# Optimization experiments

Measured on AMD Instinct MI355X. Metric: run time of the kernel, lower is better.

## Reference

```python
import jax, jax.numpy as jnp
import numpy as np
import math

NUM_HEADS = 16
ROPE_BASE = 10000.0


def _rope_tables(T, head_dim, dtype=jnp.float32):
    pos = jnp.arange(T, dtype=jnp.float32)
    inv_freq = 1.0 / (ROPE_BASE ** (jnp.arange(0, head_dim, 2, dtype=jnp.float32) / head_dim))
    ang = pos[:, None] * inv_freq[None, :]  # (T, D/2)
    return jnp.cos(ang).astype(dtype), jnp.sin(ang).astype(dtype)


def _apply_rope(x, cos, sin):
    # x: (B, T, H, D); rotate interleaved pairs, position indexed along T
    B, T, H, D = x.shape
    xr = x.reshape(B, T, H, D // 2, 2)
    xe, xo = xr[..., 0], xr[..., 1]
    c = cos[None, :, None, :]  # (1, T, 1, D/2)
    s = sin[None, :, None, :]
    re = xe * c - xo * s
    im = xe * s + xo * c
    return jnp.stack([re, im], axis=-1).reshape(B, T, H, D)


def setup_inputs() -> dict:
    key = jax.random.key(0)
    k1, k2, k3 = jax.random.split(key, 3)
    B, T, C = 2, 2048, 1024
    x = jax.random.normal(k1, (B, T, C), dtype=jnp.float32)
    w_qkv = jax.random.normal(k2, (C, 3 * C), dtype=jnp.float32) * (1.0 / math.sqrt(C))
    w_out = jax.random.normal(k3, (C, C), dtype=jnp.float32) * (1.0 / math.sqrt(C))
    return {"x": x, "w_qkv": w_qkv, "w_out": w_out}


def reference(x, w_qkv, w_out):
    B, T, C = x.shape
    H = NUM_HEADS
    D = C // H
    qkv = jnp.einsum('btc,cf->btf', x, w_qkv)  # (B, T, 3C)
    q, k, v = jnp.split(qkv, 3, axis=-1)
    q = q.reshape(B, T, H, D)
    k = k.reshape(B, T, H, D)
    v = v.reshape(B, T, H, D)
    cos, sin = _rope_tables(T, D)
    q = _apply_rope(q, cos, sin)
    k = _apply_rope(k, cos, sin)
    # (B, H, T, T) scores with causal mask
    att = jnp.einsum('bqhd,bkhd->bhqk', q, k) * (1.0 / math.sqrt(D))
    causal = jnp.tril(jnp.ones((T, T), dtype=bool))
    att = jnp.where(causal[None, None], att, -jnp.inf)
    att = jax.nn.softmax(att, axis=-1)
    out = jnp.einsum('bhqk,bkhd->bqhd', att, v).reshape(B, T, C)
    return jnp.einsum('btc,cd->btd', out, w_out)
```

## Files before the change

### kernel.cpp

```cpp
#include <hip/hip_runtime.h>
#include <stdint.h>


#define B_ 2
#define T_ 2048
#define C_ 1024
#define H_ 16
#define D_ 64
#define F_ 3072
#define M_ 4096

typedef unsigned short u16;
typedef unsigned int u32;
typedef u16 u16x2 __attribute__((ext_vector_type(2)));
typedef u16 u16x4 __attribute__((ext_vector_type(4)));
typedef u16 u16x8 __attribute__((ext_vector_type(8)));
typedef __bf16 bf16x4 __attribute__((ext_vector_type(4)));
typedef __bf16 bf16x8 __attribute__((ext_vector_type(8)));
typedef float f32x4 __attribute__((ext_vector_type(4)));

__device__ __forceinline__ float b2f(u16 u) {
  union { unsigned int i; float f; } v; v.i = ((unsigned int)u) << 16; return v.f;
}
__device__ __forceinline__ u16 f2b(float f) {
  unsigned int u = __float_as_uint(f);
  u += 0x7fffu + ((u >> 16) & 1u);
  return (u16)(u >> 16);
}
__device__ __forceinline__ bf16x8 u2b8(u16x8 v) {
  union { u16x8 u; bf16x8 b; } x; x.u = v; return x.b;
}


__global__ __launch_bounds__(256) void rope_table_kernel(float* cosT, float* sinT) {
  int idx = blockIdx.x * 256 + threadIdx.x;
  int t = idx >> 5, i = idx & 31;
  float inv_freq = powf(10000.0f, -(float)(2 * i) / 64.0f);
  float ang = (float)t * inv_freq;
  cosT[idx] = cosf(ang);
  sinT[idx] = sinf(ang);
}

__global__ __launch_bounds__(256) void cast_x_kernel(const float* __restrict__ x,
                                                     u16* __restrict__ xb) {
  int i = blockIdx.x * 256 + threadIdx.x;
  float4 v = ((const float4*)x)[i];
  u16x4 r;
  r[0] = f2b(v.x); r[1] = f2b(v.y); r[2] = f2b(v.z); r[3] = f2b(v.w);
  ((u16x4*)xb)[i] = r;
}

__global__ __launch_bounds__(256) void transpose_cast_kernel(const float* __restrict__ in,
                                                             u16* __restrict__ out,
                                                             int R, int Ccol) {
  __shared__ float tile[32][33];
  int c0 = blockIdx.x * 32, r0 = blockIdx.y * 32;
  int tx = threadIdx.x & 31, ty = threadIdx.x >> 5;
  #pragma unroll
  for (int i = 0; i < 32; i += 8)
    tile[ty + i][tx] = in[(size_t)(r0 + ty + i) * Ccol + c0 + tx];
  __syncthreads();
  #pragma unroll
  for (int i = 0; i < 32; i += 8)
    out[(size_t)(c0 + ty + i) * R + r0 + tx] = f2b(tile[tx][ty + i]);
}

template <typename TO>
__global__ __launch_bounds__(256) void gemm_bt_kernel(const u16* __restrict__ A,
                                                      const u16* __restrict__ Bt,
                                                      TO* __restrict__ Cm,
                                                      int M, int N, int K) {
  __shared__ u16 sA[128 * 32];
  __shared__ u16 sB[128 * 32];
  const int tid = threadIdx.x;
  const int lane = tid & 63;
  const int wv = tid >> 6;
  const int wr = wv >> 1, wc = wv & 1;
  const int l16 = lane & 15, lq = lane >> 4;
  const int rowBase = blockIdx.y * 128;
  const int colBase = blockIdx.x * 128;

  f32x4 acc[4][4] = {};

  const int e0 = wv * 1024 + lane * 8;

  for (int k0 = 0; k0 < K; k0 += 32) {
    #pragma unroll
    for (int s = 0; s < 2; ++s) {
      int e = e0 + s * 512;
      int r = e >> 5, c = e & 31;
      __builtin_amdgcn_global_load_lds(
          (const __attribute__((address_space(1))) u32*)(A + (size_t)(rowBase + r) * K + k0 + c),
          (__attribute__((address_space(3))) u32*)&sA[wv * 1024 + s * 512], 16, 0, 0);
      __builtin_amdgcn_global_load_lds(
          (const __attribute__((address_space(1))) u32*)(Bt + (size_t)(colBase + r) * K + k0 + c),
          (__attribute__((address_space(3))) u32*)&sB[wv * 1024 + s * 512], 16, 0, 0);
    }
    __syncthreads();
    bf16x8 af[4], bf[4];
    #pragma unroll
    for (int m = 0; m < 4; ++m)
      af[m] = u2b8(*(const u16x8*)&sA[(wr * 64 + m * 16 + l16) * 32 + lq * 8]);
    #pragma unroll
    for (int n = 0; n < 4; ++n)
      bf[n] = u2b8(*(const u16x8*)&sB[(wc * 64 + n * 16 + l16) * 32 + lq * 8]);
    #pragma unroll
    for (int m = 0; m < 4; ++m)
      #pragma unroll
      for (int n = 0; n < 4; ++n)
        acc[m][n] = __builtin_amdgcn_mfma_f32_16x16x32_bf16(af[m], bf[n], acc[m][n], 0, 0, 0);
    __syncthreads();
  }

  #pragma unroll
  for (int m = 0; m < 4; ++m) {
    #pragma unroll
    for (int n = 0; n < 4; ++n) {
      int row = rowBase + wr * 64 + m * 16 + lq * 4;
      int col = colBase + wc * 64 + n * 16 + l16;
      #pragma unroll
      for (int j = 0; j < 4; ++j) {
        float v = acc[m][n][j];
        if constexpr (sizeof(TO) == 2) {
          Cm[(size_t)(row + j) * N + col] = f2b(v);
        } else {
          Cm[(size_t)(row + j) * N + col] = v;
        }
      }
    }
  }
}

__global__ __launch_bounds__(256) void rope_reorg_kernel(const u16* __restrict__ qkv,
                                                         const float* __restrict__ cosT,
                                                         const float* __restrict__ sinT,
                                                         u16* __restrict__ qr,
                                                         u16* __restrict__ kr,
                                                         u16* __restrict__ vr) {
  const float QSC = 0.125f * 1.44269504f;
  int idx = blockIdx.x * 256 + threadIdx.x;
  int d2 = idx & 31;
  int h = (idx >> 5) & 15;
  int t = (idx >> 9) & 2047;
  int b = idx >> 20;
  size_t base = (size_t)(b * T_ + t) * F_ + h * 64 + d2 * 2;
  float qe = b2f(qkv[base]),        qo = b2f(qkv[base + 1]);
  float ke = b2f(qkv[base + C_]),   ko = b2f(qkv[base + C_ + 1]);
  float cv = cosT[t * 32 + d2], sv = sinT[t * 32 + d2];
  size_t ob = ((size_t)(b * H_ + h) * T_ + t) * D_ + d2 * 2;
  qr[ob]     = f2b((qe * cv - qo * sv) * QSC);
  qr[ob + 1] = f2b((qe * sv + qo * cv) * QSC);
  kr[ob]     = f2b(ke * cv - ko * sv);
  kr[ob + 1] = f2b(ke * sv + ko * cv);
  vr[ob]     = qkv[base + 2 * C_];
  vr[ob + 1] = qkv[base + 2 * C_ + 1];
}

__global__ __launch_bounds__(256, 4) void attn_mfma_kernel(const u16* __restrict__ qr,
                                                           const u16* __restrict__ kr,
                                                           const u16* __restrict__ vr,
                                                           u16* __restrict__ ao) {
  constexpr int LDK = 72, LDVT = 72;
  __shared__ u16 sK[2][64 * LDK];
  __shared__ u16 sVt[2][64 * LDVT];

  const int tid = threadIdx.x;
  const int lane = tid & 63;
  const int w = tid >> 6;
  const int l16 = lane & 15, lq = lane >> 4;
  const int bh = blockIdx.x;
  const int qt = (int)gridDim.y - 1 - (int)blockIdx.y;
  const int qbase = qt * 64;
  const size_t hb = (size_t)bh * (T_ * D_);

  bf16x8 qv[2];
  #pragma unroll
  for (int dc = 0; dc < 2; ++dc) {
    int row = qbase + w * 16 + l16;
    qv[dc] = u2b8(*(const u16x8*)(qr + hb + (size_t)row * 64 + dc * 32 + lq * 8));
  }

  f32x4 o[4] = {};
  float mrow = -1e30f;
  float lrow = 0.0f;

  const int skk = tid >> 3;
  const int sd0 = (tid & 7) * 8;
  const int vkp = tid & 31;
  const int vdb = tid >> 5;
  const int vtr = ((vkp >> 4) & 1) * 32 + ((vkp >> 1) & 1) * 16 +
                  ((vkp >> 3) & 1) * 8 + ((vkp >> 2) & 1) * 4 + (vkp & 1) * 2;

  u16x8 rk0, rk1, rv0, rv1;
#define LOADKV(k0)                                                             \
  {                                                                            \
    rk0 = *(const u16x8*)(kr + hb + (size_t)((k0) + skk) * 64 + sd0);          \
    rk1 = *(const u16x8*)(kr + hb + (size_t)((k0) + 32 + skk) * 64 + sd0);     \
    rv0 = *(const u16x8*)(vr + hb + (size_t)((k0) + vtr) * 64 + vdb * 8);      \
    rv1 = *(const u16x8*)(vr + hb + (size_t)((k0) + vtr + 1) * 64 + vdb * 8);  \
  }
#define WRITEKV(buf)                                                           \
  {                                                                            \
    *(u16x8*)&sK[buf][skk * LDK + sd0] = rk0;                                  \
    *(u16x8*)&sK[buf][(32 + skk) * LDK + sd0] = rk1;                           \
    _Pragma("unroll")                                                          \
    for (int u = 0; u < 8; ++u) {                                              \
      u16x2 pk; pk[0] = rv0[u]; pk[1] = rv1[u];                                \
      *(u16x2*)&sVt[buf][(vdb * 8 + u) * LDVT + 2 * vkp] = pk;                 \
    }                                                                          \
  }

  LOADKV(0);
  WRITEKV(0);
  __syncthreads();

  const int nt = qt + 1;
  int cur = 0;
  for (int it = 0; it < nt; ++it) {
    const int k0 = it * 64;
    const bool more = (it + 1 < nt);
    if (more) LOADKV(k0 + 64);

    f32x4 accs[4] = {};
    __builtin_amdgcn_s_setprio(1);
    #pragma unroll
    for (int kt = 0; kt < 4; ++kt) {
      bf16x8 kf0 = u2b8(*(const u16x8*)&sK[cur][(kt * 16 + l16) * LDK + lq * 8]);
      bf16x8 kf1 = u2b8(*(const u16x8*)&sK[cur][(kt * 16 + l16) * LDK + 32 + lq * 8]);
      accs[kt] = __builtin_amdgcn_mfma_f32_16x16x32_bf16(kf0, qv[0], accs[kt], 0, 0, 0);
      accs[kt] = __builtin_amdgcn_mfma_f32_16x16x32_bf16(kf1, qv[1], accs[kt], 0, 0, 0);
    }
    __builtin_amdgcn_s_setprio(0);

    const int qrow = qbase + w * 16 + l16;
    if (k0 + 63 > qbase + w * 16) {
      #pragma unroll
      for (int kt = 0; kt < 4; ++kt)
        #pragma unroll
        for (int j = 0; j < 4; ++j)
          if (k0 + kt * 16 + lq * 4 + j > qrow) accs[kt][j] = -1e30f;
    }
    float m0 = fmaxf(fmaxf(accs[0][0], accs[0][1]), fmaxf(accs[0][2], accs[0][3]));
    float m1 = fmaxf(fmaxf(accs[1][0], accs[1][1]), fmaxf(accs[1][2], accs[1][3]));
    float m2 = fmaxf(fmaxf(accs[2][0], accs[2][1]), fmaxf(accs[2][2], accs[2][3]));
    float m3 = fmaxf(fmaxf(accs[3][0], accs[3][1]), fmaxf(accs[3][2], accs[3][3]));
    float mx = fmaxf(fmaxf(m0, m1), fmaxf(m2, m3));
    mx = fmaxf(mx, __shfl_xor(mx, 16));
    mx = fmaxf(mx, __shfl_xor(mx, 32));

    if (!__all(mx <= mrow)) {
      float mnew = fmaxf(mrow, mx);
      float corr = __builtin_amdgcn_exp2f(mrow - mnew);
      lrow *= corr;
      mrow = mnew;
      f32x4 corrv;
      #pragma unroll
      for (int j = 0; j < 4; ++j) corrv[j] = __shfl(corr, lq * 4 + j);
      #pragma unroll
      for (int dt = 0; dt < 4; ++dt) o[dt] *= corrv;
    }
    const float mu = mrow;
    u16x8 pb[2];
    float lsum = 0.0f;
    #pragma unroll
    for (int kt = 0; kt < 4; ++kt) {
      #pragma unroll
      for (int j = 0; j < 4; ++j) {
        float p = __builtin_amdgcn_exp2f(accs[kt][j] - mu);
        lsum += p;
        pb[kt >> 1][(kt & 1) * 4 + j] = f2b(p);
      }
    }
    lrow += lsum;

    __builtin_amdgcn_s_setprio(1);
    #pragma unroll
    for (int kc = 0; kc < 2; ++kc) {
      bf16x8 pa = u2b8(pb[kc]);
      #pragma unroll
      for (int dt = 0; dt < 4; ++dt) {
        bf16x8 vt = u2b8(*(const u16x8*)&sVt[cur][(dt * 16 + l16) * LDVT + kc * 32 + lq * 8]);
        o[dt] = __builtin_amdgcn_mfma_f32_16x16x32_bf16(pa, vt, o[dt], 0, 0, 0);
      }
    }
    __builtin_amdgcn_s_setprio(0);

    if (more) WRITEKV(cur ^ 1);
    __syncthreads();
    cur ^= 1;
  }

  const int b = bh >> 4, h = bh & 15;
  float l = lrow;
  l += __shfl_xor(l, 16);
  l += __shfl_xor(l, 32);
  float linv = 1.0f / l;
  #pragma unroll
  for (int j = 0; j < 4; ++j) {
    float lj = __shfl(linv, lq * 4 + j);
    int row = qbase + w * 16 + lq * 4 + j;
    u16* orow = ao + ((size_t)(b * T_ + row)) * C_ + h * 64;
    #pragma unroll
    for (int dt = 0; dt < 4; ++dt)
      orow[dt * 16 + l16] = f2b(o[dt][j] * lj);
  }
}

extern "C" void kernel_launch(void* const* d_in, const int* in_sizes, int n_in,
                              void* d_out, int out_size, void* d_ws, size_t ws_size,
                              hipStream_t stream) {
  const float* x     = (const float*)d_in[0];
  const float* w_qkv = (const float*)d_in[1];
  const float* w_out = (const float*)d_in[2];
  float* out = (float*)d_out;
  char* ws = (char*)d_ws;

  u16* xb     = (u16*)(ws + 0);
  u16* wqkvT  = (u16*)(ws + 8388608);
  u16* woutT  = (u16*)(ws + 14680064);
  u16* qkv    = (u16*)(ws + 16777216);
  u16* qr     = (u16*)(ws + 41943040);
  u16* kr     = (u16*)(ws + 50331648);
  u16* vr     = (u16*)(ws + 58720256);
  u16* ao     = (u16*)(ws + 67108864);
  float* cosT = (float*)(ws + 75497472);
  float* sinT = (float*)(ws + 75759616);

  rope_table_kernel<<<256, 256, 0, stream>>>(cosT, sinT);
  cast_x_kernel<<<4096, 256, 0, stream>>>(x, xb);
  transpose_cast_kernel<<<dim3(96, 32), 256, 0, stream>>>(w_qkv, wqkvT, C_, F_);
  transpose_cast_kernel<<<dim3(32, 32), 256, 0, stream>>>(w_out, woutT, C_, C_);
  gemm_bt_kernel<u16><<<dim3(F_ / 128, M_ / 128), 256, 0, stream>>>(xb, wqkvT, qkv, M_, F_, C_);
  rope_reorg_kernel<<<8192, 256, 0, stream>>>(qkv, cosT, sinT, qr, kr, vr);
  attn_mfma_kernel<<<dim3(B_ * H_, T_ / 64), 256, 0, stream>>>(qr, kr, vr, ao);
  gemm_bt_kernel<float><<<dim3(C_ / 128, M_ / 128), 256, 0, stream>>>(ao, woutT, out, M_, C_, C_);
}
```

Before: 141.2 us.

## Double-buffer GEMM LDS tiles and use native bf16 conversion for P

The GEMM kernel now keeps two LDS buffers per operand and issues the global-to-LDS loads for the next K tile before computing on the current one, waiting with partial vmcnt counts and raw barriers. This is meant to overlap memory latency with MFMA work, and it raises MFMA priority around the inner product. In the attention kernel, the manual round-to-nearest bf16 conversion of the softmax probabilities is replaced with a native __bf16 cast, which may compile to hardware conversion instructions. The cost is doubled LDS use in the GEMM, which could lower occupancy, plus reliance on hand-written waitcnt values staying correct.

```diff
diff --git a/kernel.cpp b/kernel.cpp
--- a/kernel.cpp
+++ b/kernel.cpp
@@ -15,7 +15,6 @@
 typedef u16 u16x2 __attribute__((ext_vector_type(2)));
 typedef u16 u16x4 __attribute__((ext_vector_type(4)));
 typedef u16 u16x8 __attribute__((ext_vector_type(8)));
-typedef __bf16 bf16x4 __attribute__((ext_vector_type(4)));
 typedef __bf16 bf16x8 __attribute__((ext_vector_type(8)));
 typedef float f32x4 __attribute__((ext_vector_type(4)));
 
@@ -70,8 +69,8 @@
                                                       const u16* __restrict__ Bt,
                                                       TO* __restrict__ Cm,
                                                       int M, int N, int K) {
-  __shared__ u16 sA[128 * 32];
-  __shared__ u16 sB[128 * 32];
+  __shared__ u16 sA[2][128 * 32];
+  __shared__ u16 sB[2][128 * 32];
   const int tid = threadIdx.x;
   const int lane = tid & 63;
   const int wv = tid >> 6;
@@ -84,33 +83,53 @@
 
   const int e0 = wv * 1024 + lane * 8;
 
-  for (int k0 = 0; k0 < K; k0 += 32) {
-    #pragma unroll
-    for (int s = 0; s < 2; ++s) {
-      int e = e0 + s * 512;
-      int r = e >> 5, c = e & 31;
-      __builtin_amdgcn_global_load_lds(
-          (const __attribute__((address_space(1))) u32*)(A + (size_t)(rowBase + r) * K + k0 + c),
-          (__attribute__((address_space(3))) u32*)&sA[wv * 1024 + s * 512], 16, 0, 0);
-      __builtin_amdgcn_global_load_lds(
-          (const __attribute__((address_space(1))) u32*)(Bt + (size_t)(colBase + r) * K + k0 + c),
-          (__attribute__((address_space(3))) u32*)&sB[wv * 1024 + s * 512], 16, 0, 0);
-    }
-    __syncthreads();
+#define GSTAGE(buf, kk)                                                          \
+  {                                                                              \
+    _Pragma("unroll")                                                            \
+    for (int s = 0; s < 2; ++s) {                                                \
+      int e = e0 + s * 512;                                                      \
+      int r = e >> 5, ccc = e & 31;                                              \
+      __builtin_amdgcn_global_load_lds(                                          \
+          (const __attribute__((address_space(1))) u32*)(A + (size_t)(rowBase + r) * K + (kk) + ccc), \
+          (__attribute__((address_space(3))) u32*)&sA[buf][wv * 1024 + s * 512], 16, 0, 0); \
+      __builtin_amdgcn_global_load_lds(                                          \
+          (const __attribute__((address_space(1))) u32*)(Bt + (size_t)(colBase + r) * K + (kk) + ccc), \
+          (__attribute__((address_space(3))) u32*)&sB[buf][wv * 1024 + s * 512], 16, 0, 0); \
+    }                                                                            \
+  }
+
+  GSTAGE(0, 0);
+  asm volatile("s_waitcnt vmcnt(0)" ::: "memory");
+  __builtin_amdgcn_s_barrier();
+
+  int cb = 0;
+  for (int k0 = 0; k0 < K; k0 += 32, cb ^= 1) {
+    const bool more = (k0 + 32 < K);
+    if (more) {
+      GSTAGE(cb ^ 1, k0 + 32);
+      asm volatile("s_waitcnt vmcnt(4)" ::: "memory");
+    } else {
+      asm volatile("s_waitcnt vmcnt(0)" ::: "memory");
+    }
+    __builtin_amdgcn_s_barrier();
+
     bf16x8 af[4], bf[4];
     #pragma unroll
     for (int m = 0; m < 4; ++m)
-      af[m] = u2b8(*(const u16x8*)&sA[(wr * 64 + m * 16 + l16) * 32 + lq * 8]);
+      af[m] = u2b8(*(const u16x8*)&sA[cb][(wr * 64 + m * 16 + l16) * 32 + lq * 8]);
     #pragma unroll
     for (int n = 0; n < 4; ++n)
-      bf[n] = u2b8(*(const u16x8*)&sB[(wc * 64 + n * 16 + l16) * 32 + lq * 8]);
+      bf[n] = u2b8(*(const u16x8*)&sB[cb][(wc * 64 + n * 16 + l16) * 32 + lq * 8]);
+    __builtin_amdgcn_s_setprio(1);
     #pragma unroll
     for (int m = 0; m < 4; ++m)
       #pragma unroll
       for (int n = 0; n < 4; ++n)
         acc[m][n] = __builtin_amdgcn_mfma_f32_16x16x32_bf16(af[m], bf[n], acc[m][n], 0, 0, 0);
-    __syncthreads();
-  }
+    __builtin_amdgcn_s_setprio(0);
+    __builtin_amdgcn_s_barrier();
+  }
+#undef GSTAGE
 
   #pragma unroll
   for (int m = 0; m < 4; ++m) {
@@ -260,7 +279,7 @@
       for (int dt = 0; dt < 4; ++dt) o[dt] *= corrv;
     }
     const float mu = mrow;
-    u16x8 pb[2];
+    bf16x8 pb[2];
     float lsum = 0.0f;
     #pragma unroll
     for (int kt = 0; kt < 4; ++kt) {
@@ -268,7 +287,7 @@
       for (int j = 0; j < 4; ++j) {
         float p = __builtin_amdgcn_exp2f(accs[kt][j] - mu);
         lsum += p;
-        pb[kt >> 1][(kt & 1) * 4 + j] = f2b(p);
+        pb[kt >> 1][(kt & 1) * 4 + j] = (__bf16)p;
       }
     }
     lrow += lsum;
@@ -276,11 +295,10 @@
     __builtin_amdgcn_s_setprio(1);
     #pragma unroll
     for (int kc = 0; kc < 2; ++kc) {
-      bf16x8 pa = u2b8(pb[kc]);
       #pragma unroll
       for (int dt = 0; dt < 4; ++dt) {
         bf16x8 vt = u2b8(*(const u16x8*)&sVt[cur][(dt * 16 + l16) * LDVT + kc * 32 + lq * 8]);
-        o[dt] = __builtin_amdgcn_mfma_f32_16x16x32_bf16(pa, vt, o[dt], 0, 0, 0);
+        o[dt] = __builtin_amdgcn_mfma_f32_16x16x32_bf16(pb[kc], vt, o[dt], 0, 0, 0);
       }
     }
     __builtin_amdgcn_s_setprio(0);
```

Result: faster. 133.2 us (-5.7%).
